# Performance work log

Measured on AMD Instinct MI355X. Metric: run time of the kernel, lower is better.

## Reference

```python
import jax, jax.numpy as jnp
import numpy as np

B, L1, L2 = 8, 512, 512
FULL, HID, NLVL = 2048, 1024, 8
D = HID // NLVL  # attsize_per_lvl


def setup_inputs() -> dict:
    key = jax.random.key(0)
    k1, k2, k3, k4, k5, k6 = jax.random.split(key, 6)
    x1_att = jax.random.normal(k1, (B, L1, FULL), dtype=jnp.float32)
    x2_att = jax.random.normal(k2, (B, L2, FULL), dtype=jnp.float32)
    x2 = jax.random.normal(k3, (B, L2, HID), dtype=jnp.float32)
    x2_mask = jax.random.randint(k4, (B, L2), 0, 2).astype(bool)
    # nn.Linear(full_size, hidden_size, bias=False): weight [HID, FULL]
    W = jax.random.normal(k5, (HID, FULL), dtype=jnp.float32) / np.sqrt(FULL)
    final_v = jnp.ones((HID,), dtype=jnp.float32)  # linear_final param
    return {"x1_att": x1_att, "x2_att": x2_att, "x2": x2, "x2_mask": x2_mask,
            "W": W, "final_v": final_v}


def reference(x1_att, x2_att, x2, x2_mask, W, final_v):
    # dropout is identity in eval mode
    x1_key = jax.nn.relu(jnp.einsum('blf,hf->blh', x1_att, W))            # [B,L1,HID]
    x2_key = final_v * jax.nn.relu(jnp.einsum('blf,hf->blh', x2_att, W))  # [B,L2,HID]
    x1_rep = x1_key.reshape(B, L1, NLVL, D)  # split hidden into levels
    x2_rep = x2_key.reshape(B, L2, NLVL, D)
    scores = jnp.einsum('bqnd,bknd->bnqk', x1_rep, x2_rep)  # [B,NLVL,L1,L2]
    scores = jnp.where(x2_mask[:, None, None, :], -jnp.inf, scores)
    alpha = jax.nn.softmax(scores, axis=-1)                 # softmax over len2
    x2_lvl = x2.reshape(B, L2, NLVL, D)                     # value split per level
    atten = jnp.einsum('bnqk,bknd->bqnd', alpha, x2_lvl)    # [B,L1,NLVL,D]
    return atten.reshape(B, L1, HID)
```

## Files before the change

kernel.cpp:

```cpp
#include <hip/hip_runtime.h>
#include <stdint.h>

typedef _Float16 f16;
typedef _Float16 f16x4 __attribute__((ext_vector_type(4)));
typedef _Float16 f16x8 __attribute__((ext_vector_type(8)));
typedef float f32x4 __attribute__((ext_vector_type(4)));
typedef float f32x16 __attribute__((ext_vector_type(16)));

typedef const __attribute__((address_space(1))) void* gas_ptr;
typedef __attribute__((address_space(3))) void* las_ptr;

__device__ __forceinline__ void gload16(const void* g, void* l) {
  __builtin_amdgcn_global_load_lds((gas_ptr)g, (las_ptr)l, 16, 0, 0);
}

#define OFF_A16 0u
#define OFF_W16 33554432u
#define OFF_K16 37748736u
#define OFF_VT  54525952u
#define WS_NEED 62914560u

__global__ void k_convert(const float* __restrict__ x1a, const float* __restrict__ x2a,
                          const float* __restrict__ W, f16* __restrict__ A16,
                          f16* __restrict__ W16) {
  const int NA = (8192 * 2048) / 4;
  const int NH = NA / 2;
  const int NW = (1024 * 2048) / 4;
  const int NT = NA + NW;
  for (int g = blockIdx.x * blockDim.x + threadIdx.x; g < NT; g += gridDim.x * blockDim.x) {
    if (g < NA) {
      const float* src = (g < NH) ? (x1a + 4 * (size_t)g) : (x2a + 4 * (size_t)(g - NH));
      float4 v = *(const float4*)src;
      f16x4 h; h[0] = (f16)v.x; h[1] = (f16)v.y; h[2] = (f16)v.z; h[3] = (f16)v.w;
      *((f16x4*)A16 + g) = h;
    } else {
      int gw = g - NA;
      float4 v = *((const float4*)W + gw);
      f16x4 h; h[0] = (f16)v.x; h[1] = (f16)v.y; h[2] = (f16)v.z; h[3] = (f16)v.w;
      *((f16x4*)W16 + gw) = h;
    }
  }
}

__global__ void k_transpose_v(const float* __restrict__ x2, f16* __restrict__ VT) {
  __shared__ f16 T[128 * 130];
  int bid = blockIdx.x;
  int kt = bid & 3, n = (bid >> 2) & 7, b = bid >> 5;
  int t = threadIdx.x;
  int k0 = kt * 128;
  #pragma unroll
  for (int p = 0; p < 16; ++p) {
    int kl = p * 8 + (t >> 5);
    int c4 = t & 31;
    float4 v = *(const float4*)(x2 + (size_t)(b * 512 + k0 + kl) * 1024 + n * 128 + c4 * 4);
    int d0 = c4 * 4;
    T[(d0 + 0) * 130 + kl] = (f16)v.x;
    T[(d0 + 1) * 130 + kl] = (f16)v.y;
    T[(d0 + 2) * 130 + kl] = (f16)v.z;
    T[(d0 + 3) * 130 + kl] = (f16)v.w;
  }
  __syncthreads();
  #pragma unroll
  for (int p = 0; p < 8; ++p) {
    int d = p * 16 + (t >> 4);
    int c = t & 15;
    f16x8 h;
    #pragma unroll
    for (int j = 0; j < 8; ++j) h[j] = T[d * 130 + c * 8 + j];
    *(f16x8*)(VT + (size_t)((b * 8 + n) * 128 + d) * 512 + k0 + c * 8) = h;
  }
}

__global__ void __launch_bounds__(256)
k_gemm_keys(const f16* __restrict__ A16, const f16* __restrict__ W16,
            const float* __restrict__ final_v, f16* __restrict__ K16) {
  __shared__ f16 Alds[128 * 128];
  __shared__ f16 Wlds[128 * 128];
  int bid = blockIdx.x;
  int sw = (bid & 7) * 64 + (bid >> 3);
  int mt = sw >> 3, nt = sw & 7;
  int t = threadIdx.x, l = t & 63, w = t >> 6;
  int wm = w >> 1, wn = w & 1;
  f32x16 acc[2][2];
  #pragma unroll
  for (int i = 0; i < 2; ++i)
    #pragma unroll
    for (int j = 0; j < 2; ++j)
      #pragma unroll
      for (int r = 0; r < 16; ++r) acc[i][j][r] = 0.f;
  const char* Ab = (const char*)A16 + (size_t)mt * 128 * 4096;
  const char* Wb = (const char*)W16 + (size_t)nt * 128 * 4096;
  size_t soff[8];
  #pragma unroll
  for (int i = 0; i < 8; ++i) {
    int row = (w * 8 + i) * 4 + (l >> 4);
    soff[i] = (size_t)row * 4096 + (((l & 15) ^ (row & 15)) << 4);
  }
  int g8 = l >> 5;
  int rowA = wm * 64 + (l & 31);
  int rowB = wn * 64 + (l & 31);
  int sA = rowA & 15, sB = rowB & 15;
  const char* rdA0 = (const char*)Alds + rowA * 256;
  const char* rdB0 = (const char*)Wlds + rowB * 256;
  for (int ks = 0; ks < 16; ++ks) {
    int k0b = ks * 256;
    #pragma unroll
    for (int i = 0; i < 8; ++i) {
      gload16(Ab + soff[i] + k0b, (char*)Alds + (w * 8 + i) * 1024);
      gload16(Wb + soff[i] + k0b, (char*)Wlds + (w * 8 + i) * 1024);
    }
    __syncthreads();
    f16x8 af[2][8], bf[2][8];
    #pragma unroll
    for (int mi = 0; mi < 2; ++mi)
      #pragma unroll
      for (int ks2 = 0; ks2 < 8; ++ks2) {
        af[mi][ks2] = *(const f16x8*)(rdA0 + mi * 8192 + (((ks2 * 2 + g8) ^ sA) << 4));
        bf[mi][ks2] = *(const f16x8*)(rdB0 + mi * 8192 + (((ks2 * 2 + g8) ^ sB) << 4));
      }
    #pragma unroll
    for (int ks2 = 0; ks2 < 8; ++ks2)
      #pragma unroll
      for (int mi = 0; mi < 2; ++mi)
        #pragma unroll
        for (int ni = 0; ni < 2; ++ni)
          acc[mi][ni] = __builtin_amdgcn_mfma_f32_32x32x16_f16(af[mi][ks2], bf[ni][ks2], acc[mi][ni], 0, 0, 0);
    __syncthreads();
  }
  bool isx2 = (mt >= 32);
  int c = l & 31, r2 = l >> 5;
  #pragma unroll
  for (int ni = 0; ni < 2; ++ni) {
    int col = nt * 128 + wn * 64 + ni * 32 + c;
    float fvv = isx2 ? final_v[col] : 1.0f;
    #pragma unroll
    for (int mi = 0; mi < 2; ++mi) {
      int rowbase = mt * 128 + wm * 64 + mi * 32 + 4 * r2;
      #pragma unroll
      for (int r = 0; r < 16; ++r) {
        int row = rowbase + (r & 3) + 8 * (r >> 2);
        K16[(size_t)row * 1024 + col] = (f16)(fmaxf(acc[mi][ni][r], 0.f) * fvv);
      }
    }
  }
}

__global__ void __launch_bounds__(256)
k_attn(const f16* __restrict__ K16, const f16* __restrict__ VT,
       const int* __restrict__ mask, float* __restrict__ out) {
  __shared__ f16 Qlds[64 * 128];
  __shared__ f16 Klds[64 * 128];
  __shared__ f16 Vlds[128 * 64];
  __shared__ f16 Plds[4 * 16 * 64];
  __shared__ float bias[512];
  int bid = blockIdx.x;
  int qt = bid & 7, n = (bid >> 3) & 7, b = bid >> 6;
  int t = threadIdx.x, l = t & 63, w = t >> 6;
  for (int i = t; i < 512; i += 256) bias[i] = mask[b * 512 + i] ? -1e30f : 0.0f;
  int r4 = l >> 4;
  int slot = (l & 15) << 4;
  int lg = r4 << 4;
  const char* Qg = (const char*)K16 + ((size_t)(b * 512 + qt * 64) * 1024 + n * 128) * 2;
  #pragma unroll
  for (int i = 0; i < 4; ++i) {
    int rl = w * 16 + i * 4 + r4;
    gload16(Qg + (size_t)rl * 2048 + (slot ^ ((rl & 7) << 4)),
            (char*)Qlds + (w * 16 + i * 4) * 256);
  }
  __syncthreads();
  int qrow = w * 16 + (l & 15);
  int qsz = (qrow & 7) << 4;
  f16x8 qf[4];
  #pragma unroll
  for (int kk = 0; kk < 4; ++kk)
    qf[kk] = *(const f16x8*)((const char*)Qlds + qrow * 256 + ((kk * 64 + lg) ^ qsz));
  f32x4 o[8];
  #pragma unroll
  for (int dt = 0; dt < 8; ++dt) { o[dt][0] = 0.f; o[dt][1] = 0.f; o[dt][2] = 0.f; o[dt][3] = 0.f; }
  float m_r[4], l_r[4];
  #pragma unroll
  for (int r = 0; r < 4; ++r) { m_r[r] = -1e30f; l_r[r] = 0.0f; }
  const char* Kg = (const char*)K16 + ((size_t)(4096 + b * 512) * 1024 + n * 128) * 2;
  const char* Vg = (const char*)VT + (size_t)((b * 8 + n) * 128) * 1024;
  int vr = l >> 3;
  int vslot = (l & 7) << 4;
  char* Pw = (char*)Plds + w * 2048;
  for (int kt = 0; kt < 8; ++kt) {
    #pragma unroll
    for (int i = 0; i < 4; ++i) {
      int rl = w * 16 + i * 4 + r4;
      gload16(Kg + (size_t)(kt * 64 + rl) * 2048 + (slot ^ ((rl & 7) << 4)),
              (char*)Klds + (w * 16 + i * 4) * 256);
    }
    #pragma unroll
    for (int i = 0; i < 4; ++i) {
      int dl = w * 32 + i * 8 + vr;
      gload16(Vg + (size_t)dl * 1024 + kt * 128 + (vslot ^ ((dl & 7) << 4)),
              (char*)Vlds + (w * 32 + i * 8) * 128);
    }
    __syncthreads();
    f32x4 s[4];
    #pragma unroll
    for (int nt4 = 0; nt4 < 4; ++nt4) {
      s[nt4][0] = 0.f; s[nt4][1] = 0.f; s[nt4][2] = 0.f; s[nt4][3] = 0.f;
      int krow = nt4 * 16 + (l & 15);
      int ksz = (krow & 7) << 4;
      #pragma unroll
      for (int kk = 0; kk < 4; ++kk) {
        f16x8 kf = *(const f16x8*)((const char*)Klds + krow * 256 + ((kk * 64 + lg) ^ ksz));
        s[nt4] = __builtin_amdgcn_mfma_f32_16x16x32_f16(qf[kk], kf, s[nt4], 0, 0, 0);
      }
      float bc = bias[kt * 64 + nt4 * 16 + (l & 15)];
      #pragma unroll
      for (int r = 0; r < 4; ++r) s[nt4][r] += bc;
    }
    float pmax[4], scale[4], csum[4];
    #pragma unroll
    for (int r = 0; r < 4; ++r)
      pmax[r] = fmaxf(fmaxf(s[0][r], s[1][r]), fmaxf(s[2][r], s[3][r]));
    #pragma unroll
    for (int off = 1; off <= 8; off <<= 1) {
      #pragma unroll
      for (int r = 0; r < 4; ++r) pmax[r] = fmaxf(pmax[r], __shfl_xor(pmax[r], off));
    }
    #pragma unroll
    for (int r = 0; r < 4; ++r) {
      float mn = fmaxf(m_r[r], pmax[r]);
      scale[r] = __expf(m_r[r] - mn);
      m_r[r] = mn;
      csum[r] = 0.0f;
    }
    #pragma unroll
    for (int nt4 = 0; nt4 < 4; ++nt4) {
      #pragma unroll
      for (int r = 0; r < 4; ++r) {
        float sv = s[nt4][r];
        float p = (sv <= -1e29f) ? 0.0f : __expf(sv - m_r[r]);
        csum[r] += p;
        int prow = (r4 << 2) + r;
        int addr = prow * 128 + (((nt4 * 16 + (l & 15)) * 2) ^ ((prow & 7) << 4));
        *(f16*)(Pw + addr) = (f16)p;
      }
    }
    #pragma unroll
    for (int off = 1; off <= 8; off <<= 1) {
      #pragma unroll
      for (int r = 0; r < 4; ++r) csum[r] += __shfl_xor(csum[r], off);
    }
    #pragma unroll
    for (int r = 0; r < 4; ++r) l_r[r] = l_r[r] * scale[r] + csum[r];
    #pragma unroll
    for (int dt = 0; dt < 8; ++dt) {
      #pragma unroll
      for (int r = 0; r < 4; ++r) o[dt][r] *= scale[r];
    }
    asm volatile("s_waitcnt lgkmcnt(0)" ::: "memory");
    int prow = l & 15;
    int psz = (prow & 7) << 4;
    f16x8 pf0 = *(const f16x8*)((const char*)Pw + prow * 128 + (lg ^ psz));
    f16x8 pf1 = *(const f16x8*)((const char*)Pw + prow * 128 + ((lg + 64) ^ psz));
    #pragma unroll
    for (int dt = 0; dt < 8; ++dt) {
      int drow = dt * 16 + (l & 15);
      int dsz = (drow & 7) << 4;
      f16x8 vf0 = *(const f16x8*)((const char*)Vlds + drow * 128 + (lg ^ dsz));
      f16x8 vf1 = *(const f16x8*)((const char*)Vlds + drow * 128 + ((lg + 64) ^ dsz));
      o[dt] = __builtin_amdgcn_mfma_f32_16x16x32_f16(pf0, vf0, o[dt], 0, 0, 0);
      o[dt] = __builtin_amdgcn_mfma_f32_16x16x32_f16(pf1, vf1, o[dt], 0, 0, 0);
    }
    __syncthreads();
  }
  size_t ob = (size_t)(b * 512 + qt * 64 + w * 16 + (r4 << 2)) * 1024 + n * 128 + (l & 15);
  #pragma unroll
  for (int r = 0; r < 4; ++r) {
    float inv = 1.0f / fmaxf(l_r[r], 1e-30f);
    #pragma unroll
    for (int dt = 0; dt < 8; ++dt)
      out[ob + (size_t)r * 1024 + dt * 16] = o[dt][r] * inv;
  }
}

extern "C" void kernel_launch(void* const* d_in, const int* in_sizes, int n_in,
                              void* d_out, int out_size, void* d_ws, size_t ws_size,
                              hipStream_t stream) {
  const float* x1a = (const float*)d_in[0];
  const float* x2a = (const float*)d_in[1];
  const float* x2  = (const float*)d_in[2];
  const int*   msk = (const int*)d_in[3];
  const float* W   = (const float*)d_in[4];
  const float* fv  = (const float*)d_in[5];
  float* out = (float*)d_out;
  if (ws_size < (size_t)WS_NEED) return;
  char* ws = (char*)d_ws;
  f16* A16 = (f16*)(ws + OFF_A16);
  f16* W16 = (f16*)(ws + OFF_W16);
  f16* K16 = (f16*)(ws + OFF_K16);
  f16* VT  = (f16*)(ws + OFF_VT);
  k_convert<<<2048, 256, 0, stream>>>(x1a, x2a, W, A16, W16);
  k_transpose_v<<<256, 256, 0, stream>>>(x2, VT);
  k_gemm_keys<<<512, 256, 0, stream>>>(A16, W16, fv, K16);
  k_attn<<<512, 256, 0, stream>>>(K16, VT, msk, out);
}
```

Before: 96.40 us.

## Double-buffer K/V tiles in attention kernel and load Q directly from global

The attention kernel now keeps two LDS buffers for the K and V tiles. It issues the asynchronous global-to-LDS loads for the next key tile before computing on the current one, so memory latency overlaps with the MFMA and softmax work. The Q fragments are read straight from global memory into registers, which drops the Q LDS staging and one barrier. The trade-off is roughly double the LDS footprint per block, which may cut the number of resident blocks per CU. The loop is also fully unrolled, which raises register pressure.

```diff
diff --git a/kernel.cpp b/kernel.cpp
--- a/kernel.cpp
+++ b/kernel.cpp
@@ -148,9 +148,8 @@
 __global__ void __launch_bounds__(256)
 k_attn(const f16* __restrict__ K16, const f16* __restrict__ VT,
        const int* __restrict__ mask, float* __restrict__ out) {
-  __shared__ f16 Qlds[64 * 128];
-  __shared__ f16 Klds[64 * 128];
-  __shared__ f16 Vlds[128 * 64];
+  __shared__ f16 Klds[2 * 64 * 128];
+  __shared__ f16 Vlds[2 * 128 * 64];
   __shared__ f16 Plds[4 * 16 * 64];
   __shared__ float bias[512];
   int bid = blockIdx.x;
@@ -160,45 +159,48 @@
   int r4 = l >> 4;
   int slot = (l & 15) << 4;
   int lg = r4 << 4;
-  const char* Qg = (const char*)K16 + ((size_t)(b * 512 + qt * 64) * 1024 + n * 128) * 2;
-  #pragma unroll
-  for (int i = 0; i < 4; ++i) {
-    int rl = w * 16 + i * 4 + r4;
-    gload16(Qg + (size_t)rl * 2048 + (slot ^ ((rl & 7) << 4)),
-            (char*)Qlds + (w * 16 + i * 4) * 256);
-  }
-  __syncthreads();
-  int qrow = w * 16 + (l & 15);
-  int qsz = (qrow & 7) << 4;
-  f16x8 qf[4];
-  #pragma unroll
-  for (int kk = 0; kk < 4; ++kk)
-    qf[kk] = *(const f16x8*)((const char*)Qlds + qrow * 256 + ((kk * 64 + lg) ^ qsz));
-  f32x4 o[8];
-  #pragma unroll
-  for (int dt = 0; dt < 8; ++dt) { o[dt][0] = 0.f; o[dt][1] = 0.f; o[dt][2] = 0.f; o[dt][3] = 0.f; }
-  float m_r[4], l_r[4];
-  #pragma unroll
-  for (int r = 0; r < 4; ++r) { m_r[r] = -1e30f; l_r[r] = 0.0f; }
   const char* Kg = (const char*)K16 + ((size_t)(4096 + b * 512) * 1024 + n * 128) * 2;
   const char* Vg = (const char*)VT + (size_t)((b * 8 + n) * 128) * 1024;
   int vr = l >> 3;
   int vslot = (l & 7) << 4;
+
+#define STAGE_KV(ktv, bufsel) do {                                              \
+    _Pragma("unroll")                                                           \
+    for (int i_ = 0; i_ < 4; ++i_) {                                            \
+      int rl_ = w * 16 + i_ * 4 + r4;                                           \
+      gload16(Kg + (size_t)((ktv) * 64 + rl_) * 2048 + (slot ^ ((rl_ & 7) << 4)), \
+              (char*)Klds + (bufsel) * 16384 + (w * 16 + i_ * 4) * 256);        \
+    }                                                                           \
+    _Pragma("unroll")                                                           \
+    for (int i_ = 0; i_ < 4; ++i_) {                                            \
+      int dl_ = w * 32 + i_ * 8 + vr;                                           \
+      gload16(Vg + (size_t)dl_ * 1024 + (ktv) * 128 + (vslot ^ ((dl_ & 7) << 4)), \
+              (char*)Vlds + (bufsel) * 16384 + (w * 32 + i_ * 8) * 128);        \
+    }                                                                           \
+  } while (0)
+
+  const char* Qg = (const char*)K16 + ((size_t)(b * 512 + qt * 64) * 1024 + n * 128) * 2;
+  int qrow = w * 16 + (l & 15);
+  f16x8 qf[4];
+  #pragma unroll
+  for (int kk = 0; kk < 4; ++kk)
+    qf[kk] = *(const f16x8*)(Qg + (size_t)qrow * 2048 + kk * 64 + lg);
+  f32x4 o[8];
+  #pragma unroll
+  for (int dt = 0; dt < 8; ++dt) { o[dt][0] = 0.f; o[dt][1] = 0.f; o[dt][2] = 0.f; o[dt][3] = 0.f; }
+  float m_r[4], l_r[4];
+  #pragma unroll
+  for (int r = 0; r < 4; ++r) { m_r[r] = -1e30f; l_r[r] = 0.0f; }
   char* Pw = (char*)Plds + w * 2048;
+
+  STAGE_KV(0, 0);
+  __syncthreads();
+  #pragma unroll 8
   for (int kt = 0; kt < 8; ++kt) {
-    #pragma unroll
-    for (int i = 0; i < 4; ++i) {
-      int rl = w * 16 + i * 4 + r4;
-      gload16(Kg + (size_t)(kt * 64 + rl) * 2048 + (slot ^ ((rl & 7) << 4)),
-              (char*)Klds + (w * 16 + i * 4) * 256);
-    }
-    #pragma unroll
-    for (int i = 0; i < 4; ++i) {
-      int dl = w * 32 + i * 8 + vr;
-      gload16(Vg + (size_t)dl * 1024 + kt * 128 + (vslot ^ ((dl & 7) << 4)),
-              (char*)Vlds + (w * 32 + i * 8) * 128);
-    }
-    __syncthreads();
+    int cur = kt & 1;
+    if (kt < 7) STAGE_KV(kt + 1, cur ^ 1);
+    const char* Kl = (const char*)Klds + cur * 16384;
+    const char* Vl = (const char*)Vlds + cur * 16384;
     f32x4 s[4];
     #pragma unroll
     for (int nt4 = 0; nt4 < 4; ++nt4) {
@@ -207,7 +209,7 @@
       int ksz = (krow & 7) << 4;
       #pragma unroll
       for (int kk = 0; kk < 4; ++kk) {
-        f16x8 kf = *(const f16x8*)((const char*)Klds + krow * 256 + ((kk * 64 + lg) ^ ksz));
+        f16x8 kf = *(const f16x8*)(Kl + krow * 256 + ((kk * 64 + lg) ^ ksz));
         s[nt4] = __builtin_amdgcn_mfma_f32_16x16x32_f16(qf[kk], kf, s[nt4], 0, 0, 0);
       }
       float bc = bias[kt * 64 + nt4 * 16 + (l & 15)];
@@ -263,13 +265,14 @@
     for (int dt = 0; dt < 8; ++dt) {
       int drow = dt * 16 + (l & 15);
       int dsz = (drow & 7) << 4;
-      f16x8 vf0 = *(const f16x8*)((const char*)Vlds + drow * 128 + (lg ^ dsz));
-      f16x8 vf1 = *(const f16x8*)((const char*)Vlds + drow * 128 + ((lg + 64) ^ dsz));
+      f16x8 vf0 = *(const f16x8*)(Vl + drow * 128 + (lg ^ dsz));
+      f16x8 vf1 = *(const f16x8*)(Vl + drow * 128 + ((lg + 64) ^ dsz));
       o[dt] = __builtin_amdgcn_mfma_f32_16x16x32_f16(pf0, vf0, o[dt], 0, 0, 0);
       o[dt] = __builtin_amdgcn_mfma_f32_16x16x32_f16(pf1, vf1, o[dt], 0, 0, 0);
     }
     __syncthreads();
   }
+#undef STAGE_KV
   size_t ob = (size_t)(b * 512 + qt * 64 + w * 16 + (r4 << 2)) * 1024 + n * 128 + (l & 15);
   #pragma unroll
   for (int r = 0; r < 4; ++r) {
```

Measured after the change: 96.55 us. No clear change (+0.2%).
